# Optimization experiments

Measured on AMD Instinct MI355X. Metric: run time of the kernel, lower is better.

The kernel has to match this reference:

```python
import jax, jax.numpy as jnp
import numpy as np
from jax import lax

N_NODES = 100000
N_EDGES = 1600000
UNITS = 64
DEPTH_EMB = 12
DEPTH_PAR = 5
EPS = 1e-5


def setup_inputs() -> dict:
    key = jax.random.key(0)
    ks = jax.random.split(key, 24)
    x = jax.random.normal(ks[0], (N_NODES, 1), dtype=jnp.float32)
    edge_index = jax.random.randint(ks[1], (2, N_EDGES), 0, N_NODES, dtype=jnp.int32)
    s = 1.0 / np.sqrt(UNITS)
    # GCN conv params: first layer maps feats=1 -> 64, remaining 11 map 64 -> 64
    conv_w0 = jax.random.normal(ks[2], (1, UNITS), dtype=jnp.float32)
    conv_w = jax.random.normal(ks[3], (DEPTH_EMB - 1, UNITS, UNITS), dtype=jnp.float32) * s
    conv_b = jnp.zeros((DEPTH_EMB, UNITS), dtype=jnp.float32)
    # GraphNorm params (applied after every conv except the last)
    gn_gamma = jnp.ones((DEPTH_EMB - 1, UNITS), dtype=jnp.float32)
    gn_beta = jnp.zeros((DEPTH_EMB - 1, UNITS), dtype=jnp.float32)
    gn_alpha = jnp.ones((DEPTH_EMB - 1, UNITS), dtype=jnp.float32)
    # ParNet heads: 4 residual 64->64 linears + final 64->1
    phe_w = jax.random.normal(ks[4], (DEPTH_PAR - 1, UNITS, UNITS), dtype=jnp.float32) * s
    phe_b = jnp.zeros((DEPTH_PAR - 1, UNITS), dtype=jnp.float32)
    phe_wl = jax.random.normal(ks[5], (UNITS, 1), dtype=jnp.float32) * s
    phe_bl = jnp.zeros((1,), dtype=jnp.float32)
    heu_w = jax.random.normal(ks[6], (DEPTH_PAR - 1, UNITS, UNITS), dtype=jnp.float32) * s
    heu_b = jnp.zeros((DEPTH_PAR - 1, UNITS), dtype=jnp.float32)
    heu_wl = jax.random.normal(ks[7], (UNITS, 1), dtype=jnp.float32) * s
    heu_bl = jnp.zeros((1,), dtype=jnp.float32)
    return {"x": x, "edge_index": edge_index,
            "conv_w0": conv_w0, "conv_w": conv_w, "conv_b": conv_b,
            "gn_gamma": gn_gamma, "gn_beta": gn_beta, "gn_alpha": gn_alpha,
            "phe_w": phe_w, "phe_b": phe_b, "phe_wl": phe_wl, "phe_bl": phe_bl,
            "heu_w": heu_w, "heu_b": heu_b, "heu_wl": heu_wl, "heu_bl": heu_bl}


def _graph_norm(h, gamma, beta, alpha):
    # single-graph GraphNorm: per-feature mean over nodes, mean-scale alpha
    mean = jnp.mean(h, axis=0, keepdims=True)            # [1, C]
    hc = h - alpha * mean
    var = jnp.mean(hc * hc, axis=0, keepdims=True)       # [1, C]
    return gamma * hc * lax.rsqrt(var + EPS) + beta


def _parnet(h, ws, bs, wl, bl):
    for i in range(DEPTH_PAR - 1):
        h = jax.nn.relu(h + h @ ws[i] + bs[i])
    return jax.nn.sigmoid(h @ wl + bl)[:, 0]             # [N]


def reference(x, edge_index, conv_w0, conv_w, conv_b, gn_gamma, gn_beta, gn_alpha,
              phe_w, phe_b, phe_wl, phe_bl, heu_w, heu_b, heu_wl, heu_bl):
    n = x.shape[0]
    src, dst = edge_index[0], edge_index[1]
    # GCN symmetric normalization with self-loops
    deg = 1.0 + jax.ops.segment_sum(jnp.ones_like(src, dtype=x.dtype), dst, num_segments=n)
    dinv = lax.rsqrt(deg)                                # [N]
    norm_e = (dinv[src] * dinv[dst])[:, None]            # [E, 1]
    self_norm = (dinv * dinv)[:, None]                   # [N, 1]

    h = x
    for i in range(DEPTH_EMB):
        w = conv_w0 if i == 0 else conv_w[i - 1]
        h = h @ w                                        # [N, 64]
        agg = jax.ops.segment_sum(h[src] * norm_e, dst, num_segments=n)
        h = agg + h * self_norm + conv_b[i]
        if i < DEPTH_EMB - 1:
            h = _graph_norm(h, gn_gamma[i], gn_beta[i], gn_alpha[i])
            h = jax.nn.silu(h)

    phe = _parnet(h, phe_w, phe_b, phe_wl, phe_bl)
    heu = _parnet(h, heu_w, heu_b, heu_wl, heu_bl)
    return (phe, heu)
```

## Files before the change

kernel.cpp:

```cpp
#include <hip/hip_runtime.h>
#include <hip/hip_bf16.h>
#include <math.h>

#define UNITS 64
#define DEPTH_EMB 12
#define DEPTH_PAR 5
#define GN_EPS 1e-5f


__global__ void k_deg(const int* __restrict__ dst, int* __restrict__ cnt, int E) {
    int e = blockIdx.x * blockDim.x + threadIdx.x;
    if (e < E) atomicAdd(&cnt[dst[e]], 1);
}

__global__ void k_dinv(const int* __restrict__ cnt, float* __restrict__ dinv, int n) {
    int i = blockIdx.x * blockDim.x + threadIdx.x;
    if (i < n) dinv[i] = rsqrtf(1.0f + (float)cnt[i]);
}


__global__ void k_chunksum(const int* __restrict__ cnt, int* __restrict__ csum, int n) {
    __shared__ int sd[256];
    int base = blockIdx.x * 1024;
    int s = 0;
    for (int i = threadIdx.x; i < 1024; i += 256) {
        int idx = base + i;
        if (idx < n) s += cnt[idx];
    }
    sd[threadIdx.x] = s;
    __syncthreads();
    for (int off = 128; off > 0; off >>= 1) {
        if (threadIdx.x < off) sd[threadIdx.x] += sd[threadIdx.x + off];
        __syncthreads();
    }
    if (threadIdx.x == 0) csum[blockIdx.x] = sd[0];
}

__global__ void k_scansum(const int* __restrict__ csum, int* __restrict__ coff,
                          int* __restrict__ rowptr, int nchunks) {
    __shared__ int sd[256];
    int tid = threadIdx.x;
    int v = (tid < nchunks) ? csum[tid] : 0;
    sd[tid] = v;
    __syncthreads();
    for (int off = 1; off < 256; off <<= 1) {
        int t = (tid >= off) ? sd[tid - off] : 0;
        __syncthreads();
        sd[tid] += t;
        __syncthreads();
    }
    if (tid < nchunks) coff[tid] = sd[tid] - v;
    if (tid == 0) rowptr[0] = 0;
}

__global__ void k_scanfinal(const int* __restrict__ cnt, const int* __restrict__ coff,
                            int* __restrict__ rowptr, int n) {
    __shared__ int sd[1024];
    int base = blockIdx.x * 1024;
    int tid = threadIdx.x;
    int idx = base + tid;
    int v = (idx < n) ? cnt[idx] : 0;
    sd[tid] = v;
    __syncthreads();
    for (int off = 1; off < 1024; off <<= 1) {
        int t = (tid >= off) ? sd[tid - off] : 0;
        __syncthreads();
        sd[tid] += t;
        __syncthreads();
    }
    if (idx < n) rowptr[idx + 1] = coff[blockIdx.x] + sd[tid];
}

__global__ void k_fill(const int* __restrict__ src, const int* __restrict__ dst,
                       const float* __restrict__ dinv, const int* __restrict__ rowptr,
                       int* __restrict__ fill, int* __restrict__ srcs,
                       float* __restrict__ nes, int E) {
    int e = blockIdx.x * blockDim.x + threadIdx.x;
    if (e >= E) return;
    int s = src[e], d = dst[e];
    int p = rowptr[d] + atomicAdd(&fill[d], 1);
    srcs[p] = s;
    nes[p] = dinv[s] * dinv[d];
}


__global__ void k_l0(const float* __restrict__ x, const float* __restrict__ w0,
                     float* __restrict__ h2, int n) {
    int gid = blockIdx.x * blockDim.x + threadIdx.x;
    if (gid >= n * UNITS) return;
    int node = gid >> 6, c = gid & 63;
    h2[gid] = x[node] * w0[c];
}

template <int MODE>
__global__ void k_linear(const float* __restrict__ in, float* __restrict__ out,
                         const float* __restrict__ W, const float* __restrict__ b, int n) {
    int lane = threadIdx.x & 63;
    int wib = threadIdx.x >> 6;
    int wpb = blockDim.x >> 6;
    int gwave = blockIdx.x * wpb + wib;
    int nwaves = gridDim.x * wpb;

    float w[UNITS];
#pragma unroll
    for (int k = 0; k < UNITS; ++k) w[k] = W[k * UNITS + lane];
    float bj = (MODE == 1) ? b[lane] : 0.0f;

    for (int nd = gwave; nd < n; nd += nwaves) {
        int node = __builtin_amdgcn_readfirstlane(nd);
        const float* __restrict__ row = in + (size_t)node * UNITS;
        float a0 = 0.0f, a1 = 0.0f, a2 = 0.0f, a3 = 0.0f;
#pragma unroll
        for (int k = 0; k < UNITS; k += 4) {
            a0 = fmaf(row[k + 0], w[k + 0], a0);
            a1 = fmaf(row[k + 1], w[k + 1], a1);
            a2 = fmaf(row[k + 2], w[k + 2], a2);
            a3 = fmaf(row[k + 3], w[k + 3], a3);
        }
        float acc = (a0 + a1) + (a2 + a3);
        if (MODE == 1) {
            acc += row[lane] + bj;
            acc = fmaxf(acc, 0.0f);
        }
        out[(size_t)node * UNITS + lane] = acc;
    }
}


template <int DO_STATS>
__global__ void k_gather(const float* __restrict__ h2, float* __restrict__ h,
                         const int* __restrict__ rowptr, const int* __restrict__ srcs,
                         const float* __restrict__ nes, const float* __restrict__ dinv,
                         const float* __restrict__ b, float* __restrict__ stats, int n) {
    int lane = threadIdx.x & 63;
    int wib = threadIdx.x >> 6;
    int wpb = blockDim.x >> 6;
    int gwave = blockIdx.x * wpb + wib;
    int nwaves = gridDim.x * wpb;
    float bj = b[lane];
    float s1 = 0.0f, s2 = 0.0f;

    for (int nd = gwave; nd < n; nd += nwaves) {
        int node = __builtin_amdgcn_readfirstlane(nd);
        int beg = rowptr[node], end = rowptr[node + 1];
        float di = dinv[node];
        float acc0 = fmaf(h2[(size_t)node * UNITS + lane], di * di, bj);
        float acc1 = 0.0f, acc2 = 0.0f, acc3 = 0.0f;
        int j = beg;
        for (; j + 8 <= end; j += 8) {
            int i0 = srcs[j + 0], i1 = srcs[j + 1], i2 = srcs[j + 2], i3 = srcs[j + 3];
            int i4 = srcs[j + 4], i5 = srcs[j + 5], i6 = srcs[j + 6], i7 = srcs[j + 7];
            float w0 = nes[j + 0], w1 = nes[j + 1], w2 = nes[j + 2], w3 = nes[j + 3];
            float w4 = nes[j + 4], w5 = nes[j + 5], w6 = nes[j + 6], w7 = nes[j + 7];
            float v0 = h2[(size_t)i0 * UNITS + lane];
            float v1 = h2[(size_t)i1 * UNITS + lane];
            float v2 = h2[(size_t)i2 * UNITS + lane];
            float v3 = h2[(size_t)i3 * UNITS + lane];
            float v4 = h2[(size_t)i4 * UNITS + lane];
            float v5 = h2[(size_t)i5 * UNITS + lane];
            float v6 = h2[(size_t)i6 * UNITS + lane];
            float v7 = h2[(size_t)i7 * UNITS + lane];
            acc0 = fmaf(w0, v0, acc0);
            acc1 = fmaf(w1, v1, acc1);
            acc2 = fmaf(w2, v2, acc2);
            acc3 = fmaf(w3, v3, acc3);
            acc0 = fmaf(w4, v4, acc0);
            acc1 = fmaf(w5, v5, acc1);
            acc2 = fmaf(w6, v6, acc2);
            acc3 = fmaf(w7, v7, acc3);
        }
        for (; j + 4 <= end; j += 4) {
            int i0 = srcs[j + 0], i1 = srcs[j + 1], i2 = srcs[j + 2], i3 = srcs[j + 3];
            float w0 = nes[j + 0], w1 = nes[j + 1], w2 = nes[j + 2], w3 = nes[j + 3];
            float v0 = h2[(size_t)i0 * UNITS + lane];
            float v1 = h2[(size_t)i1 * UNITS + lane];
            float v2 = h2[(size_t)i2 * UNITS + lane];
            float v3 = h2[(size_t)i3 * UNITS + lane];
            acc0 = fmaf(w0, v0, acc0);
            acc1 = fmaf(w1, v1, acc1);
            acc2 = fmaf(w2, v2, acc2);
            acc3 = fmaf(w3, v3, acc3);
        }
        for (; j < end; ++j) acc0 = fmaf(nes[j], h2[(size_t)srcs[j] * UNITS + lane], acc0);
        float acc = (acc0 + acc1) + (acc2 + acc3);
        h[(size_t)node * UNITS + lane] = acc;
        if (DO_STATS) {
            s1 += acc;
            s2 = fmaf(acc, acc, s2);
        }
    }

    if (DO_STATS) {
        __shared__ float sd[2][4][UNITS];
        sd[0][wib][lane] = s1;
        sd[1][wib][lane] = s2;
        __syncthreads();
        if (threadIdx.x < UNITS) {
            float a1 = 0.0f, a2 = 0.0f;
            for (int r = 0; r < wpb; ++r) {
                a1 += sd[0][r][lane];
                a2 += sd[1][r][lane];
            }
            atomicAdd(&stats[lane], a1);
            atomicAdd(&stats[UNITS + lane], a2);
        }
    }
}


__global__ void k_norm_silu(float4* __restrict__ h, const float* __restrict__ stats,
                            const float* __restrict__ gamma, const float* __restrict__ beta,
                            const float* __restrict__ alpha, float inv_n, int total4) {
    int tid = blockIdx.x * blockDim.x + threadIdx.x;
    int c = (tid & 15) << 2;
    float A[4], Bc[4];
#pragma unroll
    for (int q = 0; q < 4; ++q) {
        float m = stats[c + q] * inv_n;
        float ex2 = stats[UNITS + c + q] * inv_n;
        float a = alpha[c + q];
        float var = ex2 - m * m * (2.0f * a - a * a);
        float g = gamma[c + q] * rsqrtf(var + GN_EPS);
        A[q] = g;
        Bc[q] = beta[c + q] - g * a * m;
    }
    int stride = gridDim.x * blockDim.x;
    for (int gid = tid; gid < total4; gid += stride) {
        float4 v = h[gid];
        float t0 = fmaf(v.x, A[0], Bc[0]);
        float t1 = fmaf(v.y, A[1], Bc[1]);
        float t2 = fmaf(v.z, A[2], Bc[2]);
        float t3 = fmaf(v.w, A[3], Bc[3]);
        v.x = t0 / (1.0f + expf(-t0));
        v.y = t1 / (1.0f + expf(-t1));
        v.z = t2 / (1.0f + expf(-t2));
        v.w = t3 / (1.0f + expf(-t3));
        h[gid] = v;
    }
}


__global__ void k_head(const float* __restrict__ in, const float* __restrict__ wl,
                       const float* __restrict__ bl, float* __restrict__ out, int n) {
    int lane = threadIdx.x & 63;
    int wib = threadIdx.x >> 6;
    int wpb = blockDim.x >> 6;
    int gwave = blockIdx.x * wpb + wib;
    int nwaves = gridDim.x * wpb;
    float wv = wl[lane];
    float blv = bl[0];
    for (int node = gwave; node < n; node += nwaves) {
        float p = in[(size_t)node * UNITS + lane] * wv;
#pragma unroll
        for (int off = 32; off > 0; off >>= 1) p += __shfl_xor(p, off, 64);
        if (lane == 0) out[node] = 1.0f / (1.0f + expf(-(p + blv)));
    }
}


extern "C" void kernel_launch(void* const* d_in, const int* in_sizes, int n_in,
                              void* d_out, int out_size, void* d_ws, size_t ws_size,
                              hipStream_t stream) {
    const float* x = (const float*)d_in[0];
    const int* ei = (const int*)d_in[1];
    const float* conv_w0 = (const float*)d_in[2];
    const float* conv_w = (const float*)d_in[3];
    const float* conv_b = (const float*)d_in[4];
    const float* gn_gamma = (const float*)d_in[5];
    const float* gn_beta = (const float*)d_in[6];
    const float* gn_alpha = (const float*)d_in[7];
    const float* phe_w = (const float*)d_in[8];
    const float* phe_b = (const float*)d_in[9];
    const float* phe_wl = (const float*)d_in[10];
    const float* phe_bl = (const float*)d_in[11];
    const float* heu_w = (const float*)d_in[12];
    const float* heu_b = (const float*)d_in[13];
    const float* heu_wl = (const float*)d_in[14];
    const float* heu_bl = (const float*)d_in[15];

    const int N = in_sizes[0];
    const int E = in_sizes[1] / 2;
    const int NC = N * UNITS;
    const int NCHUNK = (N + 1023) / 1024;

    const int* src = ei;
    const int* dstp = ei + E;

    char* w = (char*)d_ws;
    float* dinv = (float*)w;  w += (size_t)N * 4;
    float* nes = (float*)w;   w += (size_t)E * 4;
    float* h = (float*)w;     w += (size_t)NC * 4;
    float* h2 = (float*)w;    w += (size_t)NC * 4;
    float* h3 = (float*)w;    w += (size_t)NC * 4;
    float* stats = (float*)w; w += 128 * 4;
    int* cnt = (int*)w;       w += (size_t)N * 4;
    int* rowptr = (int*)w;    w += (size_t)(N + 1) * 4;
    int* fillc = (int*)w;     w += (size_t)N * 4;
    int* srcs = (int*)w;      w += (size_t)E * 4;
    int* csum = (int*)w;      w += 256 * 4;
    int* coff = (int*)w;      w += 256 * 4;

    float* out = (float*)d_out;

    const int B = 256;
    const int gE = (E + B - 1) / B;
    const int gN = (N + B - 1) / B;
    const int gNC = (NC + B - 1) / B;

    hipMemsetAsync(cnt, 0, (size_t)N * 4, stream);
    hipMemsetAsync(fillc, 0, (size_t)N * 4, stream);
    k_deg<<<gE, B, 0, stream>>>(dstp, cnt, E);
    k_dinv<<<gN, B, 0, stream>>>(cnt, dinv, N);
    k_chunksum<<<NCHUNK, 256, 0, stream>>>(cnt, csum, N);
    k_scansum<<<1, 256, 0, stream>>>(csum, coff, rowptr, NCHUNK);
    k_scanfinal<<<NCHUNK, 1024, 0, stream>>>(cnt, coff, rowptr, N);
    k_fill<<<gE, B, 0, stream>>>(src, dstp, dinv, rowptr, fillc, srcs, nes, E);

    for (int i = 0; i < DEPTH_EMB; ++i) {
        if (i == 0) {
            k_l0<<<gNC, B, 0, stream>>>(x, conv_w0, h2, N);
        } else {
            k_linear<0><<<2048, B, 0, stream>>>(h, h2, conv_w + (size_t)(i - 1) * UNITS * UNITS,
                                                nullptr, N);
        }
        int do_stats = (i < DEPTH_EMB - 1) ? 1 : 0;
        if (do_stats) {
            hipMemsetAsync(stats, 0, 128 * 4, stream);
            k_gather<1><<<2048, B, 0, stream>>>(h2, h, rowptr, srcs, nes, dinv,
                                                conv_b + (size_t)i * UNITS, stats, N);
            k_norm_silu<<<2048, B, 0, stream>>>((float4*)h, stats,
                                                gn_gamma + (size_t)i * UNITS,
                                                gn_beta + (size_t)i * UNITS,
                                                gn_alpha + (size_t)i * UNITS,
                                                1.0f / (float)N, NC / 4);
        } else {
            k_gather<0><<<2048, B, 0, stream>>>(h2, h, rowptr, srcs, nes, dinv,
                                                conv_b + (size_t)i * UNITS, stats, N);
        }
    }

    for (int head = 0; head < 2; ++head) {
        const float* wsrc = head == 0 ? phe_w : heu_w;
        const float* bsrc = head == 0 ? phe_b : heu_b;
        const float* wl = head == 0 ? phe_wl : heu_wl;
        const float* bl = head == 0 ? phe_bl : heu_bl;
        float* o = out + (size_t)head * N;

        const float* cur = h;
        float* nxt = h2;
        for (int l = 0; l < DEPTH_PAR - 1; ++l) {
            k_linear<1><<<2048, B, 0, stream>>>(cur, nxt, wsrc + (size_t)l * UNITS * UNITS,
                                                bsrc + (size_t)l * UNITS, N);
            cur = nxt;
            nxt = (nxt == h2) ? h3 : h2;
        }
        k_head<<<2048, B, 0, stream>>>(cur, wl, bl, o, N);
    }
}
```

Baseline: 1.891 ms.

## Store pre-scaled features in fp16 and fold GCN norm into node-side dinv

The linear layer now multiplies its output by the source node's dinv and stores it as fp16. The gather can then sum neighbour rows without per-edge weights and apply the destination's dinv plus bias once per node. This removes the per-edge nes array and halves the bytes of every random row gather, which is the dominant memory traffic. It also swaps expf for the fast __expf in SiLU and the sigmoid head. The cost is fp16 rounding of intermediate features, which may affect accuracy.

```diff
diff --git a/kernel.cpp b/kernel.cpp
--- a/kernel.cpp
+++ b/kernel.cpp
@@ -1,5 +1,6 @@
 #include <hip/hip_runtime.h>
 #include <hip/hip_bf16.h>
+#include <hip/hip_fp16.h>
 #include <math.h>
 
 #define UNITS 64
@@ -72,29 +73,26 @@
 }
 
 __global__ void k_fill(const int* __restrict__ src, const int* __restrict__ dst,
-                       const float* __restrict__ dinv, const int* __restrict__ rowptr,
-                       int* __restrict__ fill, int* __restrict__ srcs,
-                       float* __restrict__ nes, int E) {
+                       const int* __restrict__ rowptr, int* __restrict__ fill,
+                       int* __restrict__ srcs, int E) {
     int e = blockIdx.x * blockDim.x + threadIdx.x;
     if (e >= E) return;
     int s = src[e], d = dst[e];
     int p = rowptr[d] + atomicAdd(&fill[d], 1);
     srcs[p] = s;
-    nes[p] = dinv[s] * dinv[d];
 }
 
 
 __global__ void k_l0(const float* __restrict__ x, const float* __restrict__ w0,
-                     float* __restrict__ h2, int n) {
+                     const float* __restrict__ dinv, __half* __restrict__ h2, int n) {
     int gid = blockIdx.x * blockDim.x + threadIdx.x;
     if (gid >= n * UNITS) return;
     int node = gid >> 6, c = gid & 63;
-    h2[gid] = x[node] * w0[c];
-}
-
-template <int MODE>
-__global__ void k_linear(const float* __restrict__ in, float* __restrict__ out,
-                         const float* __restrict__ W, const float* __restrict__ b, int n) {
+    h2[gid] = __float2half(x[node] * w0[c] * dinv[node]);
+}
+
+__global__ void k_linear_emb(const float* __restrict__ in, __half* __restrict__ out,
+                             const float* __restrict__ W, const float* __restrict__ dinv, int n) {
     int lane = threadIdx.x & 63;
     int wib = threadIdx.x >> 6;
     int wpb = blockDim.x >> 6;
@@ -104,11 +102,11 @@
     float w[UNITS];
 #pragma unroll
     for (int k = 0; k < UNITS; ++k) w[k] = W[k * UNITS + lane];
-    float bj = (MODE == 1) ? b[lane] : 0.0f;
 
     for (int nd = gwave; nd < n; nd += nwaves) {
         int node = __builtin_amdgcn_readfirstlane(nd);
         const float* __restrict__ row = in + (size_t)node * UNITS;
+        float di = dinv[node];
         float a0 = 0.0f, a1 = 0.0f, a2 = 0.0f, a3 = 0.0f;
 #pragma unroll
         for (int k = 0; k < UNITS; k += 4) {
@@ -118,20 +116,46 @@
             a3 = fmaf(row[k + 3], w[k + 3], a3);
         }
         float acc = (a0 + a1) + (a2 + a3);
-        if (MODE == 1) {
-            acc += row[lane] + bj;
-            acc = fmaxf(acc, 0.0f);
-        }
+        out[(size_t)node * UNITS + lane] = __float2half(acc * di);
+    }
+}
+
+__global__ void k_linear_par(const float* __restrict__ in, float* __restrict__ out,
+                             const float* __restrict__ W, const float* __restrict__ b, int n) {
+    int lane = threadIdx.x & 63;
+    int wib = threadIdx.x >> 6;
+    int wpb = blockDim.x >> 6;
+    int gwave = blockIdx.x * wpb + wib;
+    int nwaves = gridDim.x * wpb;
+
+    float w[UNITS];
+#pragma unroll
+    for (int k = 0; k < UNITS; ++k) w[k] = W[k * UNITS + lane];
+    float bj = b[lane];
+
+    for (int nd = gwave; nd < n; nd += nwaves) {
+        int node = __builtin_amdgcn_readfirstlane(nd);
+        const float* __restrict__ row = in + (size_t)node * UNITS;
+        float a0 = 0.0f, a1 = 0.0f, a2 = 0.0f, a3 = 0.0f;
+#pragma unroll
+        for (int k = 0; k < UNITS; k += 4) {
+            a0 = fmaf(row[k + 0], w[k + 0], a0);
+            a1 = fmaf(row[k + 1], w[k + 1], a1);
+            a2 = fmaf(row[k + 2], w[k + 2], a2);
+            a3 = fmaf(row[k + 3], w[k + 3], a3);
+        }
+        float acc = (a0 + a1) + (a2 + a3) + row[lane] + bj;
+        acc = fmaxf(acc, 0.0f);
         out[(size_t)node * UNITS + lane] = acc;
     }
 }
 
 
 template <int DO_STATS>
-__global__ void k_gather(const float* __restrict__ h2, float* __restrict__ h,
+__global__ void k_gather(const __half* __restrict__ h2, float* __restrict__ h,
                          const int* __restrict__ rowptr, const int* __restrict__ srcs,
-                         const float* __restrict__ nes, const float* __restrict__ dinv,
-                         const float* __restrict__ b, float* __restrict__ stats, int n) {
+                         const float* __restrict__ dinv, const float* __restrict__ b,
+                         float* __restrict__ stats, int n) {
     int lane = threadIdx.x & 63;
     int wib = threadIdx.x >> 6;
     int wpb = blockDim.x >> 6;
@@ -144,49 +168,38 @@
         int node = __builtin_amdgcn_readfirstlane(nd);
         int beg = rowptr[node], end = rowptr[node + 1];
         float di = dinv[node];
-        float acc0 = fmaf(h2[(size_t)node * UNITS + lane], di * di, bj);
+        float acc0 = __half2float(h2[(size_t)node * UNITS + lane]);
         float acc1 = 0.0f, acc2 = 0.0f, acc3 = 0.0f;
         int j = beg;
         for (; j + 8 <= end; j += 8) {
             int i0 = srcs[j + 0], i1 = srcs[j + 1], i2 = srcs[j + 2], i3 = srcs[j + 3];
             int i4 = srcs[j + 4], i5 = srcs[j + 5], i6 = srcs[j + 6], i7 = srcs[j + 7];
-            float w0 = nes[j + 0], w1 = nes[j + 1], w2 = nes[j + 2], w3 = nes[j + 3];
-            float w4 = nes[j + 4], w5 = nes[j + 5], w6 = nes[j + 6], w7 = nes[j + 7];
-            float v0 = h2[(size_t)i0 * UNITS + lane];
-            float v1 = h2[(size_t)i1 * UNITS + lane];
-            float v2 = h2[(size_t)i2 * UNITS + lane];
-            float v3 = h2[(size_t)i3 * UNITS + lane];
-            float v4 = h2[(size_t)i4 * UNITS + lane];
-            float v5 = h2[(size_t)i5 * UNITS + lane];
-            float v6 = h2[(size_t)i6 * UNITS + lane];
-            float v7 = h2[(size_t)i7 * UNITS + lane];
-            acc0 = fmaf(w0, v0, acc0);
-            acc1 = fmaf(w1, v1, acc1);
-            acc2 = fmaf(w2, v2, acc2);
-            acc3 = fmaf(w3, v3, acc3);
-            acc0 = fmaf(w4, v4, acc0);
-            acc1 = fmaf(w5, v5, acc1);
-            acc2 = fmaf(w6, v6, acc2);
-            acc3 = fmaf(w7, v7, acc3);
+            float v0 = __half2float(h2[(size_t)i0 * UNITS + lane]);
+            float v1 = __half2float(h2[(size_t)i1 * UNITS + lane]);
+            float v2 = __half2float(h2[(size_t)i2 * UNITS + lane]);
+            float v3 = __half2float(h2[(size_t)i3 * UNITS + lane]);
+            float v4 = __half2float(h2[(size_t)i4 * UNITS + lane]);
+            float v5 = __half2float(h2[(size_t)i5 * UNITS + lane]);
+            float v6 = __half2float(h2[(size_t)i6 * UNITS + lane]);
+            float v7 = __half2float(h2[(size_t)i7 * UNITS + lane]);
+            acc0 += v0; acc1 += v1; acc2 += v2; acc3 += v3;
+            acc0 += v4; acc1 += v5; acc2 += v6; acc3 += v7;
         }
         for (; j + 4 <= end; j += 4) {
             int i0 = srcs[j + 0], i1 = srcs[j + 1], i2 = srcs[j + 2], i3 = srcs[j + 3];
-            float w0 = nes[j + 0], w1 = nes[j + 1], w2 = nes[j + 2], w3 = nes[j + 3];
-            float v0 = h2[(size_t)i0 * UNITS + lane];
-            float v1 = h2[(size_t)i1 * UNITS + lane];
-            float v2 = h2[(size_t)i2 * UNITS + lane];
-            float v3 = h2[(size_t)i3 * UNITS + lane];
-            acc0 = fmaf(w0, v0, acc0);
-            acc1 = fmaf(w1, v1, acc1);
-            acc2 = fmaf(w2, v2, acc2);
-            acc3 = fmaf(w3, v3, acc3);
-        }
-        for (; j < end; ++j) acc0 = fmaf(nes[j], h2[(size_t)srcs[j] * UNITS + lane], acc0);
+            float v0 = __half2float(h2[(size_t)i0 * UNITS + lane]);
+            float v1 = __half2float(h2[(size_t)i1 * UNITS + lane]);
+            float v2 = __half2float(h2[(size_t)i2 * UNITS + lane]);
+            float v3 = __half2float(h2[(size_t)i3 * UNITS + lane]);
+            acc0 += v0; acc1 += v1; acc2 += v2; acc3 += v3;
+        }
+        for (; j < end; ++j) acc0 += __half2float(h2[(size_t)srcs[j] * UNITS + lane]);
         float acc = (acc0 + acc1) + (acc2 + acc3);
-        h[(size_t)node * UNITS + lane] = acc;
+        float hv = fmaf(acc, di, bj);
+        h[(size_t)node * UNITS + lane] = hv;
         if (DO_STATS) {
-            s1 += acc;
-            s2 = fmaf(acc, acc, s2);
+            s1 += hv;
+            s2 = fmaf(hv, hv, s2);
         }
     }
 
@@ -231,10 +244,10 @@
         float t1 = fmaf(v.y, A[1], Bc[1]);
         float t2 = fmaf(v.z, A[2], Bc[2]);
         float t3 = fmaf(v.w, A[3], Bc[3]);
-        v.x = t0 / (1.0f + expf(-t0));
-        v.y = t1 / (1.0f + expf(-t1));
-        v.z = t2 / (1.0f + expf(-t2));
-        v.w = t3 / (1.0f + expf(-t3));
+        v.x = t0 / (1.0f + __expf(-t0));
+        v.y = t1 / (1.0f + __expf(-t1));
+        v.z = t2 / (1.0f + __expf(-t2));
+        v.w = t3 / (1.0f + __expf(-t3));
         h[gid] = v;
     }
 }
@@ -253,7 +266,7 @@
         float p = in[(size_t)node * UNITS + lane] * wv;
 #pragma unroll
         for (int off = 32; off > 0; off >>= 1) p += __shfl_xor(p, off, 64);
-        if (lane == 0) out[node] = 1.0f / (1.0f + expf(-(p + blv)));
+        if (lane == 0) out[node] = 1.0f / (1.0f + __expf(-(p + blv)));
     }
 }
 
@@ -288,9 +301,8 @@
 
     char* w = (char*)d_ws;
     float* dinv = (float*)w;  w += (size_t)N * 4;
-    float* nes = (float*)w;   w += (size_t)E * 4;
     float* h = (float*)w;     w += (size_t)NC * 4;
-    float* h2 = (float*)w;    w += (size_t)NC * 4;
+    float* hx = (float*)w;    w += (size_t)NC * 4;
     float* h3 = (float*)w;    w += (size_t)NC * 4;
     float* stats = (float*)w; w += 128 * 4;
     int* cnt = (int*)w;       w += (size_t)N * 4;
@@ -300,6 +312,7 @@
     int* csum = (int*)w;      w += 256 * 4;
     int* coff = (int*)w;      w += 256 * 4;
 
+    __half* h2 = (__half*)hx;
     float* out = (float*)d_out;
 
     const int B = 256;
@@ -314,19 +327,19 @@
     k_chunksum<<<NCHUNK, 256, 0, stream>>>(cnt, csum, N);
     k_scansum<<<1, 256, 0, stream>>>(csum, coff, rowptr, NCHUNK);
     k_scanfinal<<<NCHUNK, 1024, 0, stream>>>(cnt, coff, rowptr, N);
-    k_fill<<<gE, B, 0, stream>>>(src, dstp, dinv, rowptr, fillc, srcs, nes, E);
+    k_fill<<<gE, B, 0, stream>>>(src, dstp, rowptr, fillc, srcs, E);
 
     for (int i = 0; i < DEPTH_EMB; ++i) {
         if (i == 0) {
-            k_l0<<<gNC, B, 0, stream>>>(x, conv_w0, h2, N);
+            k_l0<<<gNC, B, 0, stream>>>(x, conv_w0, dinv, h2, N);
         } else {
-            k_linear<0><<<2048, B, 0, stream>>>(h, h2, conv_w + (size_t)(i - 1) * UNITS * UNITS,
-                                                nullptr, N);
+            k_linear_emb<<<2048, B, 0, stream>>>(h, h2, conv_w + (size_t)(i - 1) * UNITS * UNITS,
+                                                 dinv, N);
         }
         int do_stats = (i < DEPTH_EMB - 1) ? 1 : 0;
         if (do_stats) {
             hipMemsetAsync(stats, 0, 128 * 4, stream);
-            k_gather<1><<<2048, B, 0, stream>>>(h2, h, rowptr, srcs, nes, dinv,
+            k_gather<1><<<2048, B, 0, stream>>>(h2, h, rowptr, srcs, dinv,
                                                 conv_b + (size_t)i * UNITS, stats, N);
             k_norm_silu<<<2048, B, 0, stream>>>((float4*)h, stats,
                                                 gn_gamma + (size_t)i * UNITS,
@@ -334,7 +347,7 @@
                                                 gn_alpha + (size_t)i * UNITS,
                                                 1.0f / (float)N, NC / 4);
         } else {
-            k_gather<0><<<2048, B, 0, stream>>>(h2, h, rowptr, srcs, nes, dinv,
+            k_gather<0><<<2048, B, 0, stream>>>(h2, h, rowptr, srcs, dinv,
                                                 conv_b + (size_t)i * UNITS, stats, N);
         }
     }
@@ -347,12 +360,12 @@
         float* o = out + (size_t)head * N;
 
         const float* cur = h;
-        float* nxt = h2;
+        float* nxt = h3;
         for (int l = 0; l < DEPTH_PAR - 1; ++l) {
-            k_linear<1><<<2048, B, 0, stream>>>(cur, nxt, wsrc + (size_t)l * UNITS * UNITS,
-                                                bsrc + (size_t)l * UNITS, N);
+            k_linear_par<<<2048, B, 0, stream>>>(cur, nxt, wsrc + (size_t)l * UNITS * UNITS,
+                                                 bsrc + (size_t)l * UNITS, N);
             cur = nxt;
-            nxt = (nxt == h2) ? h3 : h2;
+            nxt = (nxt == h3) ? hx : h3;
         }
         k_head<<<2048, B, 0, stream>>>(cur, wl, bl, o, N);
     }
```

Measured after the change: 1.707 ms. 9.7% less time.
